# Optimization experiments

Measured on AMD Instinct MI355X. Metric: run time of the kernel, lower is better.

## Reference

```python
import jax, jax.numpy as jnp
import numpy as np

MAX_DISP = 9
STRIDE = 1


def setup_inputs() -> dict:
    key = jax.random.key(0)
    kA, kB = jax.random.split(key)
    N, Z, H, W = 8, 128, 160, 160
    imgA = jax.random.normal(kA, (N, Z, H, W), dtype=jnp.float32)
    imgB = jax.random.normal(kB, (N, Z, H, W), dtype=jnp.float32)
    return {"imgA": imgA, "imgB": imgB}


def _corr_volume(imgA, imgB, max_disp, stride):
    N, Z, H, W = imgA.shape
    center = (max_disp + 1) / 2 - 1  # = 4.0 for max_disp=9
    # base sampling grid in [-1, 1] (align_corners=True convention)
    sx = jnp.linspace(-1.0, 1.0, W)[None, :]  # [1, W] -> x coord
    sy = jnp.linspace(-1.0, 1.0, H)[:, None]  # [H, 1] -> y coord
    # winsize = i * max_disp + j with i -> x-offset (scaled by 2/(H-1)),
    # j -> y-offset (scaled by 2/(W-1)), exactly as in the torch code.
    ks = jnp.arange(max_disp ** 2)
    dxs = (2.0 / (H - 1)) * ((ks // max_disp).astype(jnp.float32) - center) * stride
    dys = (2.0 / (W - 1)) * ((ks % max_disp).astype(jnp.float32) - center) * stride

    def sample_dot(carry, d):
        dx, dy = d
        # normalized grid -> pixel coords (align_corners=True)
        x = jnp.broadcast_to((sx + dx + 1.0) * 0.5 * (W - 1), (H, W))
        y = jnp.broadcast_to((sy + dy + 1.0) * 0.5 * (H - 1), (H, W))
        x0 = jnp.floor(x).astype(jnp.int32)
        y0 = jnp.floor(y).astype(jnp.int32)
        x1, y1 = x0 + 1, y0 + 1
        wx1 = x - x0.astype(x.dtype)
        wy1 = y - y0.astype(y.dtype)
        wx0, wy0 = 1.0 - wx1, 1.0 - wy1

        def corner(yi, xi, w):
            valid = (xi >= 0) & (xi < W) & (yi >= 0) & (yi < H)  # zeros padding
            xc = jnp.clip(xi, 0, W - 1)
            yc = jnp.clip(yi, 0, H - 1)
            return imgB[:, :, yc, xc] * jnp.where(valid, w, 0.0)  # [N,Z,H,W]

        sampled = (corner(y0, x0, wy0 * wx0) + corner(y0, x1, wy0 * wx1)
                   + corner(y1, x0, wy1 * wx0) + corner(y1, x1, wy1 * wx1))
        corr = jnp.einsum('nzhw,nzhw->nhw', imgA, sampled)  # channel dot
        return carry, corr

    _, corrs = jax.lax.scan(sample_dot, None, (dxs, dys))  # [81, N, H, W]
    return jnp.transpose(corrs, (1, 0, 2, 3))  # [N, 81, H, W]


def reference(imgA, imgB):
    return _corr_volume(imgA, imgB, MAX_DISP, STRIDE)
```

## Files before the change

kernel.cpp:

```cpp
#include <hip/hip_runtime.h>

#define NB 8
#define ZD 128
#define HD 160
#define WD 160
#define TI 16
#define TJ 32
#define ZC 2
#define NCHUNK (ZD / ZC)
#define BR (TI + 8)
#define ASL 9
#define BSL 11
#define A_SLOTS (ZC * TI * ASL)
#define B_SLOTS (ZC * BR * BSL)
#define BUF_SLOTS 832
#define NBUF 3
#define NTHREADS 576
#define CHUNK_ELEMS (ZC * HD * WD)

#define GP(x) ((const __attribute__((address_space(1))) void*)(x))
#define LP(x) ((__attribute__((address_space(3))) void*)(x))

__global__ __launch_bounds__(NTHREADS, 4)
void corr_vol_kernel(const float* __restrict__ A, const float* __restrict__ B,
                     const float* __restrict__ zp, float* __restrict__ out) {
    __shared__ float4 lds[NBUF * BUF_SLOTS];
    __shared__ float4 dump[64];

    const int tid = threadIdx.x;
    const int bid = blockIdx.x;
    const int jt = bid % 5;
    const int it = (bid / 5) % 10;
    const int n  = bid / 50;
    const int i0 = it * TI;
    const int j0 = jt * TJ;

    const float* Abase = A + (size_t)n * ZD * HD * WD;
    const float* Bbase = B + (size_t)n * ZD * HD * WD;

    const float* p1; int st1;
    if (tid < A_SLOTS) {
        const int a = tid, zA = a / (TI * ASL), rA = (a / ASL) % TI, cA = a % ASL;
        const bool v = (cA < 8);
        p1 = v ? (Abase + ((size_t)zA * HD + (i0 + rA)) * WD + j0 + 4 * cA) : zp;
        st1 = v ? CHUNK_ELEMS : 0;
    } else {
        const int q = tid - A_SLOTS;
        const int z = q / (BR * BSL), rw = (q / BSL) % BR, c = q % BSL;
        const int gr = i0 + rw - 4, gc = j0 + 4 * c - 4;
        const bool v = (c < 10) && ((unsigned)gr < (unsigned)HD) && ((unsigned)gc < (unsigned)WD);
        p1 = v ? (Bbase + ((size_t)z * HD + gr) * WD + gc) : zp;
        st1 = v ? CHUNK_ELEMS : 0;
    }
    const int s2 = tid + NTHREADS;
    const int q2 = s2 - A_SLOTS;
    const int z2 = q2 / (BR * BSL), rw2 = (q2 / BSL) % BR, c2 = q2 % BSL;
    const int gr2 = i0 + rw2 - 4, gc2 = j0 + 4 * c2 - 4;
    const bool v2 = (q2 < B_SLOTS) && (c2 < 10) &&
                    ((unsigned)gr2 < (unsigned)HD) && ((unsigned)gc2 < (unsigned)WD);
    const float* p2 = v2 ? (Bbase + ((size_t)z2 * HD + gr2) * WD + gc2) : zp;
    const int st2 = v2 ? CHUNK_ELEMS : 0;
    const bool s2_in = (s2 < BUF_SLOTS);
    const unsigned d1 = (unsigned)(tid & ~63);
    const unsigned d2 = (unsigned)(s2 & ~63);

    auto prefetch = [&](int k2, int pb) {
        if (k2 < NCHUNK) {
            char* base = (char*)&lds[pb * BUF_SLOTS];
            __builtin_amdgcn_global_load_lds(GP(p1 + (size_t)k2 * st1),
                                             LP(base + 16u * d1), 16, 0, 0);
            __builtin_amdgcn_global_load_lds(GP(p2 + (size_t)k2 * st2),
                                             LP(s2_in ? (base + 16u * d2) : (char*)&dump[0]), 16, 0, 0);
        } else {
            __builtin_amdgcn_global_load_lds(GP(zp), LP((char*)&dump[0]), 16, 0, 0);
            __builtin_amdgcn_global_load_lds(GP(zp), LP((char*)&dump[0]), 16, 0, 0);
        }
    };

    const int w = tid >> 6;
    const int l = tid & 63;
    const int g = l & 3;
    const int r = l >> 2;

    float acc[9][8];
    #pragma unroll
    for (int d = 0; d < 9; ++d)
        #pragma unroll
        for (int p = 0; p < 8; ++p) acc[d][p] = 0.f;

    prefetch(0, 0);
    prefetch(1, 1);

    for (int k = 0; k < NCHUNK; ++k) {
        asm volatile("s_waitcnt vmcnt(2)\n\ts_barrier" ::: "memory");
        prefetch(k + 2, (k + 2) % 3);

        const float* Af = (const float*)&lds[(k % 3) * BUF_SLOTS];
        const float* Bf = Af + 4 * A_SLOTS;
        #pragma unroll
        for (int z = 0; z < ZC; ++z) {
            float a[8], b[16];
            const float* ap = Af + z * (TI * ASL * 4) + r * (ASL * 4) + 8 * g;
            const float* bp = Bf + z * (BR * BSL * 4) + (r + w) * (BSL * 4) + 8 * g;
            *(float4*)&a[0] = *(const float4*)&ap[0];
            *(float4*)&a[4] = *(const float4*)&ap[4];
            *(float4*)&b[0]  = *(const float4*)&bp[0];
            *(float4*)&b[4]  = *(const float4*)&bp[4];
            *(float4*)&b[8]  = *(const float4*)&bp[8];
            *(float4*)&b[12] = *(const float4*)&bp[12];
            #pragma unroll
            for (int d = 0; d < 9; ++d)
                #pragma unroll
                for (int p = 0; p < 8; ++p)
                    acc[d][p] = fmaf(a[p], b[p + d], acc[d][p]);
        }
    }
    asm volatile("s_waitcnt vmcnt(0)" ::: "memory");

    float* obase = out + (((size_t)n * 81) * HD + (i0 + r)) * WD + j0 + 8 * g;
    #pragma unroll
    for (int d = 0; d < 9; ++d) {
        const int kk = d * 9 + w;
        float* o = obase + (size_t)kk * HD * WD;
        *(float4*)&o[0] = make_float4(acc[d][0], acc[d][1], acc[d][2], acc[d][3]);
        *(float4*)&o[4] = make_float4(acc[d][4], acc[d][5], acc[d][6], acc[d][7]);
    }
}

extern "C" void kernel_launch(void* const* d_in, const int* in_sizes, int n_in,
                              void* d_out, int out_size, void* d_ws, size_t ws_size,
                              hipStream_t stream) {
    const float* A = (const float*)d_in[0];
    const float* B = (const float*)d_in[1];
    float* out = (float*)d_out;
    hipMemsetAsync(d_ws, 0, 256, stream);
    corr_vol_kernel<<<dim3(NB * 10 * 5), dim3(NTHREADS), 0, stream>>>(
        A, B, (const float*)d_ws, out);
}
```

Before: 354.0 us.

## Replace LDS staging with direct register double-buffered global loads, split displacements across blocks

Drops the triple-buffered async global-to-LDS pipeline and barriers. Each thread now loads its A and B vectors straight from global memory into registers, double-buffered across channels. The 9 displacement rows are split across 3 blocks of 192 threads instead of one 576-thread block, and block IDs are swizzled across the 8 images. This removes barrier and LDS traffic and adds blocks, but every wave reloads overlapping B rows from global/L2, which raises cache traffic.

Measured after the change: 431.6 us. 1.22x slower.

```diff
diff --git a/kernel.cpp b/kernel.cpp
--- a/kernel.cpp
+++ b/kernel.cpp
@@ -4,83 +4,73 @@
 #define ZD 128
 #define HD 160
 #define WD 160
+#define PLANE (HD * WD)
+#define IMG (ZD * PLANE)
+
 #define TI 16
 #define TJ 32
-#define ZC 2
-#define NCHUNK (ZD / ZC)
-#define BR (TI + 8)
-#define ASL 9
-#define BSL 11
-#define A_SLOTS (ZC * TI * ASL)
-#define B_SLOTS (ZC * BR * BSL)
-#define BUF_SLOTS 832
-#define NBUF 3
-#define NTHREADS 576
-#define CHUNK_ELEMS (ZC * HD * WD)
+#define TILES_PER_IMG 50
+#define DQ 3
+#define NTHREADS 192
 
-#define GP(x) ((const __attribute__((address_space(1))) void*)(x))
-#define LP(x) ((__attribute__((address_space(3))) void*)(x))
+#define LOADS(aa, bb) do { \
+    *(float4*)(&aa[0])  = *(const float4*)(pa); \
+    *(float4*)(&aa[4])  = *(const float4*)(pa + 4); \
+    *(float4*)(&bb[0])  = *(const float4*)(pb0); \
+    *(float4*)(&bb[4])  = *(const float4*)(pb1); \
+    *(float4*)(&bb[8])  = *(const float4*)(pb2); \
+    *(float4*)(&bb[12]) = *(const float4*)(pb3); \
+    pa += PLANE; pb0 += s0; pb1 += s1; pb2 += s2; pb3 += s3; \
+} while (0)
 
-__global__ __launch_bounds__(NTHREADS, 4)
+#define FMAS(aa, bb) do { \
+    _Pragma("unroll") \
+    for (int d = 0; d < 9; ++d) { \
+        _Pragma("unroll") \
+        for (int p = 0; p < 8; ++p) \
+            acc[d][p] = fmaf(aa[p], bb[p + d], acc[d][p]); \
+    } \
+} while (0)
+
+__global__ __launch_bounds__(NTHREADS, 3)
 void corr_vol_kernel(const float* __restrict__ A, const float* __restrict__ B,
                      const float* __restrict__ zp, float* __restrict__ out) {
-    __shared__ float4 lds[NBUF * BUF_SLOTS];
-    __shared__ float4 dump[64];
+    const int bid = blockIdx.x;
+    const int x  = bid & 7;
+    const int s  = bid >> 3;
+    const int tl = s / DQ;
+    const int dq = s - DQ * tl;
+    const int tile = x * TILES_PER_IMG + tl;
+    const int n  = tile / TILES_PER_IMG;
+    const int t2 = tile - n * TILES_PER_IMG;
+    const int it = t2 / 5, jt = t2 - 5 * it;
+    const int i0 = it * TI, j0 = jt * TJ;
 
-    const int tid = threadIdx.x;
-    const int bid = blockIdx.x;
-    const int jt = bid % 5;
-    const int it = (bid / 5) % 10;
-    const int n  = bid / 50;
-    const int i0 = it * TI;
-    const int j0 = jt * TJ;
+    const int w = dq * 3 + (threadIdx.x >> 6);
+    const int l = threadIdx.x & 63;
+    const int r = l >> 2;
+    const int g = l & 3;
 
-    const float* Abase = A + (size_t)n * ZD * HD * WD;
-    const float* Bbase = B + (size_t)n * ZD * HD * WD;
+    const float* pa = A + (size_t)n * IMG + (size_t)(i0 + r) * WD + (j0 + 8 * g);
 
-    const float* p1; int st1;
-    if (tid < A_SLOTS) {
-        const int a = tid, zA = a / (TI * ASL), rA = (a / ASL) % TI, cA = a % ASL;
-        const bool v = (cA < 8);
-        p1 = v ? (Abase + ((size_t)zA * HD + (i0 + rA)) * WD + j0 + 4 * cA) : zp;
-        st1 = v ? CHUNK_ELEMS : 0;
-    } else {
-        const int q = tid - A_SLOTS;
-        const int z = q / (BR * BSL), rw = (q / BSL) % BR, c = q % BSL;
-        const int gr = i0 + rw - 4, gc = j0 + 4 * c - 4;
-        const bool v = (c < 10) && ((unsigned)gr < (unsigned)HD) && ((unsigned)gc < (unsigned)WD);
-        p1 = v ? (Bbase + ((size_t)z * HD + gr) * WD + gc) : zp;
-        st1 = v ? CHUNK_ELEMS : 0;
+    const int br = i0 + r + w - 4;
+    const bool rv = (unsigned)br < (unsigned)HD;
+    const float* bbase = B + (size_t)n * IMG + (size_t)br * WD + (j0 + 8 * g - 4);
+    const int c0 = j0 + 8 * g - 4;
+
+    const float *pb0, *pb1, *pb2, *pb3;
+    int s0, s1, s2, s3;
+    {
+        bool v;
+        v = rv && ((unsigned)(c0 +  0) < (unsigned)WD);
+        pb0 = v ? bbase +  0 : zp;  s0 = v ? PLANE : 0;
+        v = rv && ((unsigned)(c0 +  4) < (unsigned)WD);
+        pb1 = v ? bbase +  4 : zp;  s1 = v ? PLANE : 0;
+        v = rv && ((unsigned)(c0 +  8) < (unsigned)WD);
+        pb2 = v ? bbase +  8 : zp;  s2 = v ? PLANE : 0;
+        v = rv && ((unsigned)(c0 + 12) < (unsigned)WD);
+        pb3 = v ? bbase + 12 : zp;  s3 = v ? PLANE : 0;
     }
-    const int s2 = tid + NTHREADS;
-    const int q2 = s2 - A_SLOTS;
-    const int z2 = q2 / (BR * BSL), rw2 = (q2 / BSL) % BR, c2 = q2 % BSL;
-    const int gr2 = i0 + rw2 - 4, gc2 = j0 + 4 * c2 - 4;
-    const bool v2 = (q2 < B_SLOTS) && (c2 < 10) &&
-                    ((unsigned)gr2 < (unsigned)HD) && ((unsigned)gc2 < (unsigned)WD);
-    const float* p2 = v2 ? (Bbase + ((size_t)z2 * HD + gr2) * WD + gc2) : zp;
-    const int st2 = v2 ? CHUNK_ELEMS : 0;
-    const bool s2_in = (s2 < BUF_SLOTS);
-    const unsigned d1 = (unsigned)(tid & ~63);
-    const unsigned d2 = (unsigned)(s2 & ~63);
-
-    auto prefetch = [&](int k2, int pb) {
-        if (k2 < NCHUNK) {
-            char* base = (char*)&lds[pb * BUF_SLOTS];
-            __builtin_amdgcn_global_load_lds(GP(p1 + (size_t)k2 * st1),
-                                             LP(base + 16u * d1), 16, 0, 0);
-            __builtin_amdgcn_global_load_lds(GP(p2 + (size_t)k2 * st2),
-                                             LP(s2_in ? (base + 16u * d2) : (char*)&dump[0]), 16, 0, 0);
-        } else {
-            __builtin_amdgcn_global_load_lds(GP(zp), LP((char*)&dump[0]), 16, 0, 0);
-            __builtin_amdgcn_global_load_lds(GP(zp), LP((char*)&dump[0]), 16, 0, 0);
-        }
-    };
-
-    const int w = tid >> 6;
-    const int l = tid & 63;
-    const int g = l & 3;
-    const int r = l >> 2;
 
     float acc[9][8];
     #pragma unroll
@@ -88,42 +78,27 @@
         #pragma unroll
         for (int p = 0; p < 8; ++p) acc[d][p] = 0.f;
 
-    prefetch(0, 0);
-    prefetch(1, 1);
+    float a0[8], b0[16], a1[8], b1[16];
+    LOADS(a0, b0);
+    LOADS(a1, b1);
 
-    for (int k = 0; k < NCHUNK; ++k) {
-        asm volatile("s_waitcnt vmcnt(2)\n\ts_barrier" ::: "memory");
-        prefetch(k + 2, (k + 2) % 3);
-
-        const float* Af = (const float*)&lds[(k % 3) * BUF_SLOTS];
-        const float* Bf = Af + 4 * A_SLOTS;
-        #pragma unroll
-        for (int z = 0; z < ZC; ++z) {
-            float a[8], b[16];
-            const float* ap = Af + z * (TI * ASL * 4) + r * (ASL * 4) + 8 * g;
-            const float* bp = Bf + z * (BR * BSL * 4) + (r + w) * (BSL * 4) + 8 * g;
-            *(float4*)&a[0] = *(const float4*)&ap[0];
-            *(float4*)&a[4] = *(const float4*)&ap[4];
-            *(float4*)&b[0]  = *(const float4*)&bp[0];
-            *(float4*)&b[4]  = *(const float4*)&bp[4];
-            *(float4*)&b[8]  = *(const float4*)&bp[8];
-            *(float4*)&b[12] = *(const float4*)&bp[12];
-            #pragma unroll
-            for (int d = 0; d < 9; ++d)
-                #pragma unroll
-                for (int p = 0; p < 8; ++p)
-                    acc[d][p] = fmaf(a[p], b[p + d], acc[d][p]);
-        }
+    #pragma unroll 1
+    for (int z = 0; z < ZD - 2; z += 2) {
+        FMAS(a0, b0);
+        LOADS(a0, b0);
+        FMAS(a1, b1);
+        LOADS(a1, b1);
     }
-    asm volatile("s_waitcnt vmcnt(0)" ::: "memory");
+    FMAS(a0, b0);
+    FMAS(a1, b1);
 
     float* obase = out + (((size_t)n * 81) * HD + (i0 + r)) * WD + j0 + 8 * g;
     #pragma unroll
     for (int d = 0; d < 9; ++d) {
         const int kk = d * 9 + w;
-        float* o = obase + (size_t)kk * HD * WD;
-        *(float4*)&o[0] = make_float4(acc[d][0], acc[d][1], acc[d][2], acc[d][3]);
-        *(float4*)&o[4] = make_float4(acc[d][4], acc[d][5], acc[d][6], acc[d][7]);
+        float* o = obase + (size_t)kk * PLANE;
+        *(float4*)(&o[0]) = make_float4(acc[d][0], acc[d][1], acc[d][2], acc[d][3]);
+        *(float4*)(&o[4]) = make_float4(acc[d][4], acc[d][5], acc[d][6], acc[d][7]);
     }
 }
 
@@ -134,6 +109,6 @@
     const float* B = (const float*)d_in[1];
     float* out = (float*)d_out;
     hipMemsetAsync(d_ws, 0, 256, stream);
-    corr_vol_kernel<<<dim3(NB * 10 * 5), dim3(NTHREADS), 0, stream>>>(
+    corr_vol_kernel<<<dim3(NB * TILES_PER_IMG * DQ), dim3(NTHREADS), 0, stream>>>(
         A, B, (const float*)d_ws, out);
 }
```
